# Performance work log

Measured on AMD Instinct MI355X. Metric: run time of the kernel, lower is better.

Reference implementation:

```python
import jax, jax.numpy as jnp
import numpy as np

N_NODES = 50000
N_EDGES = 600000
IN_CH = 128
OUT_CH = 64
HID = 2 * OUT_CH  # 128


def setup_inputs() -> dict:
    key = jax.random.key(0)
    k1, k2, k3, k4 = jax.random.split(key, 4)
    x = jax.random.normal(k1, (N_NODES, IN_CH), dtype=jnp.float32)
    edge_index = jax.random.randint(k2, (2, N_EDGES), 0, N_NODES, dtype=jnp.int64)
    # Glorot-style init scale for linear weights (PyG GCNConv default init)
    W1 = jax.random.normal(k3, (IN_CH, HID), dtype=jnp.float32) * (1.0 / np.sqrt(IN_CH))
    b1 = jnp.zeros((HID,), dtype=jnp.float32)
    W2 = jax.random.normal(k4, (HID, OUT_CH), dtype=jnp.float32) * (1.0 / np.sqrt(HID))
    b2 = jnp.zeros((OUT_CH,), dtype=jnp.float32)
    return {"x": x, "edge_index": edge_index, "W1": W1, "b1": b1, "W2": W2, "b2": b2}


def _gcn_norm(edge_index, n_nodes):
    # Add self loops, then symmetric normalization: norm_e = d^-1/2[src] * d^-1/2[dst]
    loop = jnp.arange(n_nodes, dtype=edge_index.dtype)
    src = jnp.concatenate([edge_index[0], loop])
    dst = jnp.concatenate([edge_index[1], loop])
    deg = jax.ops.segment_sum(jnp.ones_like(dst, dtype=jnp.float32), dst, num_segments=n_nodes)
    dinv = jnp.where(deg > 0, jax.lax.rsqrt(deg), 0.0)
    norm = dinv[src] * dinv[dst]  # [E + N]
    return src, dst, norm


def _gcn_conv(x, src, dst, norm, W, b, n_nodes):
    h = x @ W                      # [N, d_out]  dense transform first (PyG order)
    msg = h[src] * norm[:, None]   # gather + scale: [E+N, d_out]
    agg = jax.ops.segment_sum(msg, dst, num_segments=n_nodes)  # scatter-add
    return agg + b


def reference(x, edge_index, W1, b1, W2, b2):
    n = x.shape[0]
    src, dst, norm = _gcn_norm(edge_index, n)  # shared (cached=True in original)
    h = jax.nn.relu(_gcn_conv(x, src, dst, norm, W1, b1, n))
    return _gcn_conv(h, src, dst, norm, W2, b2, n)
```

## Files before the change

### kernel.cpp

```cpp
#include <hip/hip_runtime.h>


typedef __attribute__((ext_vector_type(8))) short short8;
typedef __attribute__((ext_vector_type(4))) float float4v;

constexpr int PB = 128;

static __device__ __forceinline__ ushort f2bf(float f) {
  union { float f; unsigned u; } c; c.f = f;
  unsigned u = c.u;
  return (ushort)((u + 0x7fffu + ((u >> 16) & 1u)) >> 16);
}
static __device__ __forceinline__ float bf2f(ushort h) {
  union { unsigned u; float f; } c; c.u = ((unsigned)h) << 16;
  return c.f;
}
static __device__ __forceinline__ float bfhi(unsigned packed) {
  union { unsigned u; float f; } c; c.u = packed & 0xffff0000u;
  return c.f;
}
static __device__ __forceinline__ float bflo(unsigned packed) {
  union { unsigned u; float f; } c; c.u = packed << 16;
  return c.f;
}

static __device__ __forceinline__ void wswz_tile(const float* __restrict__ W,
                                                 ushort* __restrict__ whi,
                                                 ushort* __restrict__ wlo,
                                                 int M, int tile, int lane) {
  int ntiles = M >> 4;
  int kt = tile / ntiles, nt = tile % ntiles;
  int colg = nt * 16 + (lane & 15);
  int krow = kt * 32 + (lane >> 4) * 8;
  size_t o = ((size_t)tile * 64 + lane) * 8;
#pragma unroll
  for (int j = 0; j < 8; j++) {
    float v = W[(size_t)(krow + j) * M + colg];
    ushort h = f2bf(v);
    whi[o + j] = h;
    wlo[o + j] = f2bf(v - bf2f(h));
  }
}

static __device__ __forceinline__ void lds_scan512(const int* __restrict__ g, int m,
                                                   int* __restrict__ base,
                                                   int* __restrict__ buf) {
  int t = threadIdx.x;
  int carry = 0;
  for (int b0 = 0; b0 < 512; b0 += 256) {
    int idx = b0 + t;
    int v = (idx < m) ? g[idx] : 0;
    buf[t] = v;
    __syncthreads();
    for (int off = 1; off < 256; off <<= 1) {
      int add = (t >= off) ? buf[t - off] : 0;
      __syncthreads();
      buf[t] += add;
      __syncthreads();
    }
    base[idx] = carry + buf[t] - v;
    carry += buf[255];
    __syncthreads();
  }
}

__global__ __launch_bounds__(256) void k_p1(const int* __restrict__ dst, int E, int EPB,
                                            int NBK, int* __restrict__ cnt_mat,
                                            const float* __restrict__ W1,
                                            ushort* __restrict__ w1hi,
                                            ushort* __restrict__ w1lo,
                                            const float* __restrict__ W2,
                                            ushort* __restrict__ w2hi,
                                            ushort* __restrict__ w2lo) {
  __shared__ int hist[512];
  int b = blockIdx.x, t = threadIdx.x;
  if (b >= PB) {
    int tile = (b - PB) * 4 + (t >> 6);
    int lane = t & 63;
    if (tile < 32) wswz_tile(W1, w1hi, w1lo, 128, tile, lane);
    else           wswz_tile(W2, w2hi, w2lo, 64, tile - 32, lane);
    return;
  }
  for (int k = t; k < NBK; k += 256) hist[k] = 0;
  __syncthreads();
  int start = b * EPB;
  int stop = min(E, start + EPB);
  for (int e = start + t * 4; e < stop; e += 1024) {
    if (e + 4 <= stop) {
      int4 d = *(const int4*)(dst + e);
      atomicAdd(&hist[d.x >> 7], 1);
      atomicAdd(&hist[d.y >> 7], 1);
      atomicAdd(&hist[d.z >> 7], 1);
      atomicAdd(&hist[d.w >> 7], 1);
    } else {
      for (int j = e; j < stop; j++) atomicAdd(&hist[dst[j] >> 7], 1);
    }
  }
  __syncthreads();
  for (int k = t; k < NBK; k += 256) cnt_mat[k * PB + b] = hist[k];
}

__global__ __launch_bounds__(256) void k_p2(int* __restrict__ cnt_mat,
                                            int* __restrict__ btot, int NBK,
                                            const float* __restrict__ Af32,
                                            const ushort* __restrict__ Whi,
                                            const ushort* __restrict__ Wlo,
                                            ushort* __restrict__ Cb, int n) {
  __shared__ int buf[256];
  int bid = blockIdx.x, t = threadIdx.x;
  if (bid < NBK) {
    int v = (t < PB) ? cnt_mat[bid * PB + t] : 0;
    buf[t] = v;
    __syncthreads();
#pragma unroll
    for (int off = 1; off < 256; off <<= 1) {
      int add = (t >= off) ? buf[t - off] : 0;
      __syncthreads();
      buf[t] += add;
      __syncthreads();
    }
    if (t < PB) cnt_mat[bid * PB + t] = buf[t] - v;
    if (t == 255) btot[bid] = buf[255];
    return;
  }
  constexpr int K = 128, M = 128, NT = M / 16;
  int lane = t & 63;
  int wv = t >> 6;
  int quad = lane >> 4, lo16 = lane & 15;
  int rowbase = (bid - NBK) * 64 + wv * 16;
  int arow = rowbase + lo16;
  bool arow_ok = arow < n;
  float4v acc[NT];
#pragma unroll
  for (int nt = 0; nt < NT; nt++) acc[nt] = (float4v){0.f, 0.f, 0.f, 0.f};
  for (int kt = 0; kt < 4; kt++) {
    short8 ahi, alo;
    float av[8];
    if (arow_ok) {
      const float* ap = Af32 + (size_t)arow * K + kt * 32 + quad * 8;
      float4 a0 = *(const float4*)ap;
      float4 a1 = *(const float4*)(ap + 4);
      av[0] = a0.x; av[1] = a0.y; av[2] = a0.z; av[3] = a0.w;
      av[4] = a1.x; av[5] = a1.y; av[6] = a1.z; av[7] = a1.w;
    } else {
#pragma unroll
      for (int j = 0; j < 8; j++) av[j] = 0.f;
    }
#pragma unroll
    for (int j = 0; j < 8; j++) {
      ushort h = f2bf(av[j]);
      ahi[j] = (short)h;
      alo[j] = (short)f2bf(av[j] - bf2f(h));
    }
    const ushort* ph = Whi + ((size_t)(kt * NT) * 64 + lane) * 8;
    const ushort* pl = Wlo + ((size_t)(kt * NT) * 64 + lane) * 8;
#pragma unroll
    for (int nt = 0; nt < NT; nt++) {
      short8 bhi = *(const short8*)(ph + nt * 512);
      short8 blo = *(const short8*)(pl + nt * 512);
      acc[nt] = __builtin_amdgcn_mfma_f32_16x16x32_bf16(ahi, bhi, acc[nt], 0, 0, 0);
      acc[nt] = __builtin_amdgcn_mfma_f32_16x16x32_bf16(alo, bhi, acc[nt], 0, 0, 0);
      acc[nt] = __builtin_amdgcn_mfma_f32_16x16x32_bf16(ahi, blo, acc[nt], 0, 0, 0);
    }
  }
#pragma unroll
  for (int nt = 0; nt < NT; nt++) {
#pragma unroll
    for (int r = 0; r < 4; r++) {
      int row = rowbase + quad * 4 + r;
      if (row < n) Cb[(size_t)row * M + nt * 16 + lo16] = f2bf(acc[nt][r]);
    }
  }
}

__global__ __launch_bounds__(256) void k_p3(const int* __restrict__ src,
                                            const int* __restrict__ dst, int E, int EPB,
                                            int NBK, const int* __restrict__ btot,
                                            const int* __restrict__ cnt_mat,
                                            unsigned* __restrict__ part) {
  __shared__ int buf[256];
  __shared__ int base[512];
  __shared__ int cur[512];
  int b = blockIdx.x, t = threadIdx.x;
  lds_scan512(btot, NBK, base, buf);
  for (int k = t; k < NBK; k += 256) cur[k] = base[k] + cnt_mat[k * PB + b];
  __syncthreads();
  int start = b * EPB, stop = min(E, start + EPB);
  for (int e = start + t * 4; e < stop; e += 1024) {
    if (e + 4 <= stop) {
      int4 s = *(const int4*)(src + e);
      int4 d = *(const int4*)(dst + e);
      int p;
      p = atomicAdd(&cur[d.x >> 7], 1); part[p] = (unsigned)s.x | ((unsigned)(d.x & 127) << 25);
      p = atomicAdd(&cur[d.y >> 7], 1); part[p] = (unsigned)s.y | ((unsigned)(d.y & 127) << 25);
      p = atomicAdd(&cur[d.z >> 7], 1); part[p] = (unsigned)s.z | ((unsigned)(d.z & 127) << 25);
      p = atomicAdd(&cur[d.w >> 7], 1); part[p] = (unsigned)s.w | ((unsigned)(d.w & 127) << 25);
    } else {
      for (int j = e; j < stop; j++) {
        int p2 = atomicAdd(&cur[dst[j] >> 7], 1);
        part[p2] = (unsigned)src[j] | ((unsigned)(dst[j] & 127) << 25);
      }
    }
  }
}

__global__ __launch_bounds__(256) void k_p4(const int* __restrict__ btot, int NBK,
                                            const unsigned* __restrict__ part,
                                            int* __restrict__ row_ptr,
                                            float* __restrict__ dinv,
                                            int* __restrict__ col, int n, int E) {
  __shared__ int buf[256];
  __shared__ int base[512];
  __shared__ int cnt[128];
  __shared__ int cur[128];
  int b = blockIdx.x, t = threadIdx.x;
  lds_scan512(btot, NBK, base, buf);
  int beg = base[b], end = base[b + 1];
  if (t < 128) cnt[t] = 0;
  __syncthreads();
  for (int e = beg + t; e < end; e += 256) atomicAdd(&cnt[part[e] >> 25], 1);
  __syncthreads();
  int v = (t < 128) ? cnt[t] : 0;
  buf[t] = v;
  __syncthreads();
#pragma unroll
  for (int off = 1; off < 256; off <<= 1) {
    int add = (t >= off) ? buf[t - off] : 0;
    __syncthreads();
    buf[t] += add;
    __syncthreads();
  }
  if (t < 128) {
    int excl = buf[t] - v;
    cur[t] = beg + excl;
    int node = b * 128 + t;
    if (node < n) {
      row_ptr[node] = beg + excl;
      dinv[node] = rsqrtf((float)(v + 1));
    }
  }
  if (b == 0 && t == 0) row_ptr[n] = E;
  __syncthreads();
  for (int e = beg + t; e < end; e += 256) {
    unsigned p = part[e];
    int pos = atomicAdd(&cur[p >> 25], 1);
    col[pos] = (int)(p & 0x01FFFFFFu);
  }
}

__global__ __launch_bounds__(256) void k_gemm2(const ushort* __restrict__ Ahi,
                                               const ushort* __restrict__ Alo,
                                               const ushort* __restrict__ Whi,
                                               const ushort* __restrict__ Wlo,
                                               ushort* __restrict__ Cb, int n) {
  constexpr int K = 128, M = 64, NT = M / 16;
  int lane = threadIdx.x & 63;
  int wv = threadIdx.x >> 6;
  int quad = lane >> 4, lo16 = lane & 15;
  int rowbase = blockIdx.x * 64 + wv * 16;
  int arow = rowbase + lo16;
  bool arow_ok = arow < n;
  float4v acc[NT];
#pragma unroll
  for (int nt = 0; nt < NT; nt++) acc[nt] = (float4v){0.f, 0.f, 0.f, 0.f};
  for (int kt = 0; kt < 4; kt++) {
    short8 ahi, alo;
    if (arow_ok) {
      size_t ao = (size_t)arow * K + kt * 32 + quad * 8;
      ahi = *(const short8*)(Ahi + ao);
      alo = *(const short8*)(Alo + ao);
    } else {
      ahi = (short8)0; alo = (short8)0;
    }
    const ushort* ph = Whi + ((size_t)(kt * NT) * 64 + lane) * 8;
    const ushort* pl = Wlo + ((size_t)(kt * NT) * 64 + lane) * 8;
#pragma unroll
    for (int nt = 0; nt < NT; nt++) {
      short8 bhi = *(const short8*)(ph + nt * 512);
      short8 blo = *(const short8*)(pl + nt * 512);
      acc[nt] = __builtin_amdgcn_mfma_f32_16x16x32_bf16(ahi, bhi, acc[nt], 0, 0, 0);
      acc[nt] = __builtin_amdgcn_mfma_f32_16x16x32_bf16(alo, bhi, acc[nt], 0, 0, 0);
      acc[nt] = __builtin_amdgcn_mfma_f32_16x16x32_bf16(ahi, blo, acc[nt], 0, 0, 0);
    }
  }
#pragma unroll
  for (int nt = 0; nt < NT; nt++) {
#pragma unroll
    for (int r = 0; r < 4; r++) {
      int row = rowbase + quad * 4 + r;
      if (row < n) Cb[(size_t)row * M + nt * 16 + lo16] = f2bf(acc[nt][r]);
    }
  }
}

template <int C, bool RELU, bool SPLIT>
__global__ __launch_bounds__(256) void k_agg(const ushort* __restrict__ Hb,
                                             const int* __restrict__ row_ptr,
                                             const int* __restrict__ col,
                                             const float* __restrict__ dinv,
                                             const float* __restrict__ bias,
                                             float* __restrict__ out,
                                             ushort* __restrict__ outhi,
                                             ushort* __restrict__ outlo, int n) {
  constexpr int VPL = C / 64;
  int lane = threadIdx.x & 63;
  int v = blockIdx.x * 4 + (threadIdx.x >> 6);
  if (v >= n) return;
  float dv = dinv[v];
  float acc0 = 0.f, acc1 = 0.f;
  auto loadp = [&](int s) -> unsigned {
    if (VPL == 2) return *(const unsigned*)(Hb + (size_t)s * C + lane * 2);
    else          return (unsigned)Hb[(size_t)s * C + lane];
  };
  {
    unsigned u = loadp(v);
    if (VPL == 2) { acc0 = dv * bflo(u); acc1 = dv * bfhi(u); }
    else          { acc0 = dv * bf2f((ushort)u); }
  }
  int beg = row_ptr[v], end = row_ptr[v + 1];
  for (int base = beg; base < end; base += 64) {
    int m = end - base;
    if (m > 64) m = 64;
    int sl = 0;
    float wl = 0.f;
    if (lane < m) {
      sl = col[base + lane];
      wl = dinv[sl];
    }
    int j = 0;
    for (; j + 8 <= m; j += 8) {
      int s[8]; float wq[8]; unsigned u[8];
#pragma unroll
      for (int q = 0; q < 8; q++) { s[q] = __shfl(sl, j + q); wq[q] = __shfl(wl, j + q); }
#pragma unroll
      for (int q = 0; q < 8; q++) u[q] = loadp(s[q]);
#pragma unroll
      for (int q = 0; q < 8; q++) {
        if (VPL == 2) {
          acc0 = fmaf(wq[q], bflo(u[q]), acc0);
          acc1 = fmaf(wq[q], bfhi(u[q]), acc1);
        } else {
          acc0 = fmaf(wq[q], bf2f((ushort)u[q]), acc0);
        }
      }
    }
    for (; j + 4 <= m; j += 4) {
      int s[4]; float wq[4]; unsigned u[4];
#pragma unroll
      for (int q = 0; q < 4; q++) { s[q] = __shfl(sl, j + q); wq[q] = __shfl(wl, j + q); }
#pragma unroll
      for (int q = 0; q < 4; q++) u[q] = loadp(s[q]);
#pragma unroll
      for (int q = 0; q < 4; q++) {
        if (VPL == 2) {
          acc0 = fmaf(wq[q], bflo(u[q]), acc0);
          acc1 = fmaf(wq[q], bfhi(u[q]), acc1);
        } else {
          acc0 = fmaf(wq[q], bf2f((ushort)u[q]), acc0);
        }
      }
    }
    for (; j < m; j++) {
      int s = __shfl(sl, j);
      float wv = __shfl(wl, j);
      unsigned u = loadp(s);
      if (VPL == 2) {
        acc0 = fmaf(wv, bflo(u), acc0);
        acc1 = fmaf(wv, bfhi(u), acc1);
      } else {
        acc0 = fmaf(wv, bf2f((ushort)u), acc0);
      }
    }
  }
  float r0 = fmaf(dv, acc0, bias[lane * VPL + 0]);
  if (RELU) r0 = fmaxf(r0, 0.f);
  if (VPL == 2) {
    float r1 = fmaf(dv, acc1, bias[lane * VPL + 1]);
    if (RELU) r1 = fmaxf(r1, 0.f);
    if (SPLIT) {
      ushort h0 = f2bf(r0), h1 = f2bf(r1);
      ushort l0 = f2bf(r0 - bf2f(h0)), l1 = f2bf(r1 - bf2f(h1));
      ((unsigned*)outhi)[(size_t)v * (C / 2) + lane] = (unsigned)h0 | ((unsigned)h1 << 16);
      ((unsigned*)outlo)[(size_t)v * (C / 2) + lane] = (unsigned)l0 | ((unsigned)l1 << 16);
    } else {
      *(float2*)&out[(size_t)v * C + lane * 2] = make_float2(r0, r1);
    }
  } else {
    if (SPLIT) {
      ushort h0 = f2bf(r0);
      outhi[(size_t)v * C + lane] = h0;
      outlo[(size_t)v * C + lane] = f2bf(r0 - bf2f(h0));
    } else {
      out[(size_t)v * C + lane] = r0;
    }
  }
}

extern "C" void kernel_launch(void* const* d_in, const int* in_sizes, int n_in,
                              void* d_out, int out_size, void* d_ws, size_t ws_size,
                              hipStream_t stream) {
  const float* x  = (const float*)d_in[0];
  const int*   ei = (const int*)d_in[1];
  const float* W1 = (const float*)d_in[2];
  const float* b1 = (const float*)d_in[3];
  const float* W2 = (const float*)d_in[4];
  const float* b2 = (const float*)d_in[5];
  int N = in_sizes[0] / 128;
  int E = in_sizes[1] / 2;
  const int* src = ei;
  const int* dst = ei + E;
  int NBK = (N + 127) / 128;
  int EPB = ((E + PB - 1) / PB + 3) & ~3;

  auto al = [](size_t v) { return (v + 255) & ~(size_t)255; };
  char* w = (char*)d_ws;
  int*      cnt_mat = (int*)w;      w += al((size_t)NBK * PB * 4);
  int*      btot    = (int*)w;      w += al((size_t)NBK * 4);
  unsigned* part    = (unsigned*)w; w += al((size_t)E * 4);
  int*      row_ptr = (int*)w;      w += al((size_t)(N + 1) * 4);
  float*    dinv    = (float*)w;    w += al((size_t)N * 4);
  int*      colv    = (int*)w;      w += al((size_t)E * 4);
  ushort*   h       = (ushort*)w;   w += al((size_t)N * 128 * 2);
  ushort*   h1hi    = (ushort*)w;   w += al((size_t)N * 128 * 2);
  ushort*   h1lo    = (ushort*)w;   w += al((size_t)N * 128 * 2);
  ushort*   h2      = (ushort*)w;   w += al((size_t)N * 64 * 2);
  ushort*   w1hi    = (ushort*)w;   w += al((size_t)128 * 128 * 2);
  ushort*   w1lo    = (ushort*)w;   w += al((size_t)128 * 128 * 2);
  ushort*   w2hi    = (ushort*)w;   w += al((size_t)128 * 64 * 2);
  ushort*   w2lo    = (ushort*)w;   w += al((size_t)128 * 64 * 2);
  float* out = (float*)d_out;

  int GB = (N + 63) / 64;

  k_p1<<<PB + 12, 256, 0, stream>>>(dst, E, EPB, NBK, cnt_mat,
                                    W1, w1hi, w1lo, W2, w2hi, w2lo);
  k_p2<<<NBK + GB, 256, 0, stream>>>(cnt_mat, btot, NBK, x, w1hi, w1lo, h, N);
  k_p3<<<PB, 256, 0, stream>>>(src, dst, E, EPB, NBK, btot, cnt_mat, part);
  k_p4<<<NBK, 256, 0, stream>>>(btot, NBK, part, row_ptr, dinv, colv, N, E);
  k_agg<128, true, true><<<(N + 3) / 4, 256, 0, stream>>>(h, row_ptr, colv, dinv, b1,
                                                          nullptr, h1hi, h1lo, N);
  k_gemm2<<<GB, 256, 0, stream>>>(h1hi, h1lo, w2hi, w2lo, h2, N);
  k_agg<64, false, false><<<(N + 3) / 4, 256, 0, stream>>>(h2, row_ptr, colv, dinv, b2,
                                                           out, nullptr, nullptr, N);
}
```

Measured before the change: 175.5 us.

## Fuse all GCN phases into one cooperative persistent kernel with grid syncs

Measured after the change: 614.7 us. 250% more time.

```diff
diff --git a/kernel.cpp b/kernel.cpp
--- a/kernel.cpp
+++ b/kernel.cpp
@@ -1,5 +1,8 @@
 #include <hip/hip_runtime.h>
-
+#include <hip/hip_cooperative_groups.h>
+
+
+namespace cg = cooperative_groups;
 
 typedef __attribute__((ext_vector_type(8))) short short8;
 typedef __attribute__((ext_vector_type(4))) float float4v;
@@ -23,6 +26,32 @@
   union { unsigned u; float f; } c; c.u = packed << 16;
   return c.f;
 }
+
+struct MegaParams {
+  const float* x;
+  const int* src;
+  const int* dst;
+  const float* W1;
+  const float* b1;
+  const float* W2;
+  const float* b2;
+  int N, E, NBK, EPB, GB, NAGG;
+  int* cnt_mat;
+  int* btot;
+  unsigned* part;
+  int* row_ptr;
+  float* dinv;
+  int* col;
+  ushort* h;
+  ushort* h1hi;
+  ushort* h1lo;
+  ushort* h2;
+  ushort* w1hi;
+  ushort* w1lo;
+  ushort* w2hi;
+  ushort* w2lo;
+  float* out;
+};
 
 static __device__ __forceinline__ void wswz_tile(const float* __restrict__ W,
                                                  ushort* __restrict__ whi,
@@ -64,72 +93,61 @@
   }
 }
 
-__global__ __launch_bounds__(256) void k_p1(const int* __restrict__ dst, int E, int EPB,
-                                            int NBK, int* __restrict__ cnt_mat,
-                                            const float* __restrict__ W1,
-                                            ushort* __restrict__ w1hi,
-                                            ushort* __restrict__ w1lo,
-                                            const float* __restrict__ W2,
-                                            ushort* __restrict__ w2hi,
-                                            ushort* __restrict__ w2lo) {
-  __shared__ int hist[512];
-  int b = blockIdx.x, t = threadIdx.x;
-  if (b >= PB) {
-    int tile = (b - PB) * 4 + (t >> 6);
+static __device__ void phase1_body(int bid, const MegaParams& P, int* smem) {
+  int t = threadIdx.x;
+  if (bid >= PB) {
+    int tile = (bid - PB) * 4 + (t >> 6);
     int lane = t & 63;
-    if (tile < 32) wswz_tile(W1, w1hi, w1lo, 128, tile, lane);
-    else           wswz_tile(W2, w2hi, w2lo, 64, tile - 32, lane);
+    if (tile < 32) wswz_tile(P.W1, P.w1hi, P.w1lo, 128, tile, lane);
+    else           wswz_tile(P.W2, P.w2hi, P.w2lo, 64, tile - 32, lane);
     return;
   }
-  for (int k = t; k < NBK; k += 256) hist[k] = 0;
-  __syncthreads();
-  int start = b * EPB;
-  int stop = min(E, start + EPB);
+  int* hist = smem;
+  for (int k = t; k < P.NBK; k += 256) hist[k] = 0;
+  __syncthreads();
+  int start = bid * P.EPB;
+  int stop = min(P.E, start + P.EPB);
   for (int e = start + t * 4; e < stop; e += 1024) {
     if (e + 4 <= stop) {
-      int4 d = *(const int4*)(dst + e);
+      int4 d = *(const int4*)(P.dst + e);
       atomicAdd(&hist[d.x >> 7], 1);
       atomicAdd(&hist[d.y >> 7], 1);
       atomicAdd(&hist[d.z >> 7], 1);
       atomicAdd(&hist[d.w >> 7], 1);
     } else {
-      for (int j = e; j < stop; j++) atomicAdd(&hist[dst[j] >> 7], 1);
-    }
-  }
-  __syncthreads();
-  for (int k = t; k < NBK; k += 256) cnt_mat[k * PB + b] = hist[k];
-}
-
-__global__ __launch_bounds__(256) void k_p2(int* __restrict__ cnt_mat,
-                                            int* __restrict__ btot, int NBK,
-                                            const float* __restrict__ Af32,
-                                            const ushort* __restrict__ Whi,
-                                            const ushort* __restrict__ Wlo,
-                                            ushort* __restrict__ Cb, int n) {
-  __shared__ int buf[256];
-  int bid = blockIdx.x, t = threadIdx.x;
-  if (bid < NBK) {
-    int v = (t < PB) ? cnt_mat[bid * PB + t] : 0;
-    buf[t] = v;
+      for (int j = e; j < stop; j++) atomicAdd(&hist[P.dst[j] >> 7], 1);
+    }
+  }
+  __syncthreads();
+  for (int k = t; k < P.NBK; k += 256) P.cnt_mat[k * PB + bid] = hist[k];
+}
+
+static __device__ void phase2_scan(int bid, const MegaParams& P, int* smem) {
+  int t = threadIdx.x;
+  int* buf = smem;
+  int v = (t < PB) ? P.cnt_mat[bid * PB + t] : 0;
+  buf[t] = v;
+  __syncthreads();
+#pragma unroll
+  for (int off = 1; off < 256; off <<= 1) {
+    int add = (t >= off) ? buf[t - off] : 0;
     __syncthreads();
-#pragma unroll
-    for (int off = 1; off < 256; off <<= 1) {
-      int add = (t >= off) ? buf[t - off] : 0;
-      __syncthreads();
-      buf[t] += add;
-      __syncthreads();
-    }
-    if (t < PB) cnt_mat[bid * PB + t] = buf[t] - v;
-    if (t == 255) btot[bid] = buf[255];
-    return;
-  }
+    buf[t] += add;
+    __syncthreads();
+  }
+  if (t < PB) P.cnt_mat[bid * PB + t] = buf[t] - v;
+  if (t == 255) P.btot[bid] = buf[255];
+}
+
+static __device__ void gemm1_block(int gb, const MegaParams& P) {
   constexpr int K = 128, M = 128, NT = M / 16;
+  int t = threadIdx.x;
   int lane = t & 63;
   int wv = t >> 6;
   int quad = lane >> 4, lo16 = lane & 15;
-  int rowbase = (bid - NBK) * 64 + wv * 16;
+  int rowbase = gb * 64 + wv * 16;
   int arow = rowbase + lo16;
-  bool arow_ok = arow < n;
+  bool arow_ok = arow < P.N;
   float4v acc[NT];
 #pragma unroll
   for (int nt = 0; nt < NT; nt++) acc[nt] = (float4v){0.f, 0.f, 0.f, 0.f};
@@ -137,7 +155,7 @@
     short8 ahi, alo;
     float av[8];
     if (arow_ok) {
-      const float* ap = Af32 + (size_t)arow * K + kt * 32 + quad * 8;
+      const float* ap = P.x + (size_t)arow * K + kt * 32 + quad * 8;
       float4 a0 = *(const float4*)ap;
       float4 a1 = *(const float4*)(ap + 4);
       av[0] = a0.x; av[1] = a0.y; av[2] = a0.z; av[3] = a0.w;
@@ -148,12 +166,12 @@
     }
 #pragma unroll
     for (int j = 0; j < 8; j++) {
-      ushort h = f2bf(av[j]);
-      ahi[j] = (short)h;
-      alo[j] = (short)f2bf(av[j] - bf2f(h));
-    }
-    const ushort* ph = Whi + ((size_t)(kt * NT) * 64 + lane) * 8;
-    const ushort* pl = Wlo + ((size_t)(kt * NT) * 64 + lane) * 8;
+      ushort hh = f2bf(av[j]);
+      ahi[j] = (short)hh;
+      alo[j] = (short)f2bf(av[j] - bf2f(hh));
+    }
+    const ushort* ph = P.w1hi + ((size_t)(kt * NT) * 64 + lane) * 8;
+    const ushort* pl = P.w1lo + ((size_t)(kt * NT) * 64 + lane) * 8;
 #pragma unroll
     for (int nt = 0; nt < NT; nt++) {
       short8 bhi = *(const short8*)(ph + nt * 512);
@@ -168,57 +186,49 @@
 #pragma unroll
     for (int r = 0; r < 4; r++) {
       int row = rowbase + quad * 4 + r;
-      if (row < n) Cb[(size_t)row * M + nt * 16 + lo16] = f2bf(acc[nt][r]);
-    }
-  }
-}
-
-__global__ __launch_bounds__(256) void k_p3(const int* __restrict__ src,
-                                            const int* __restrict__ dst, int E, int EPB,
-                                            int NBK, const int* __restrict__ btot,
-                                            const int* __restrict__ cnt_mat,
-                                            unsigned* __restrict__ part) {
-  __shared__ int buf[256];
-  __shared__ int base[512];
-  __shared__ int cur[512];
-  int b = blockIdx.x, t = threadIdx.x;
-  lds_scan512(btot, NBK, base, buf);
-  for (int k = t; k < NBK; k += 256) cur[k] = base[k] + cnt_mat[k * PB + b];
-  __syncthreads();
-  int start = b * EPB, stop = min(E, start + EPB);
+      if (row < P.N) P.h[(size_t)row * M + nt * 16 + lo16] = f2bf(acc[nt][r]);
+    }
+  }
+}
+
+static __device__ void phase3_body(int bid, const MegaParams& P, int* smem) {
+  int t = threadIdx.x;
+  int* buf = smem;
+  int* base = smem + 256;
+  int* cur = smem + 768;
+  lds_scan512(P.btot, P.NBK, base, buf);
+  for (int k = t; k < P.NBK; k += 256) cur[k] = base[k] + P.cnt_mat[k * PB + bid];
+  __syncthreads();
+  int start = bid * P.EPB, stop = min(P.E, start + P.EPB);
   for (int e = start + t * 4; e < stop; e += 1024) {
     if (e + 4 <= stop) {
-      int4 s = *(const int4*)(src + e);
-      int4 d = *(const int4*)(dst + e);
+      int4 s = *(const int4*)(P.src + e);
+      int4 d = *(const int4*)(P.dst + e);
       int p;
-      p = atomicAdd(&cur[d.x >> 7], 1); part[p] = (unsigned)s.x | ((unsigned)(d.x & 127) << 25);
-      p = atomicAdd(&cur[d.y >> 7], 1); part[p] = (unsigned)s.y | ((unsigned)(d.y & 127) << 25);
-      p = atomicAdd(&cur[d.z >> 7], 1); part[p] = (unsigned)s.z | ((unsigned)(d.z & 127) << 25);
-      p = atomicAdd(&cur[d.w >> 7], 1); part[p] = (unsigned)s.w | ((unsigned)(d.w & 127) << 25);
+      p = atomicAdd(&cur[d.x >> 7], 1); P.part[p] = (unsigned)s.x | ((unsigned)(d.x & 127) << 25);
+      p = atomicAdd(&cur[d.y >> 7], 1); P.part[p] = (unsigned)s.y | ((unsigned)(d.y & 127) << 25);
+      p = atomicAdd(&cur[d.z >> 7], 1); P.part[p] = (unsigned)s.z | ((unsigned)(d.z & 127) << 25);
+      p = atomicAdd(&cur[d.w >> 7], 1); P.part[p] = (unsigned)s.w | ((unsigned)(d.w & 127) << 25);
     } else {
       for (int j = e; j < stop; j++) {
-        int p2 = atomicAdd(&cur[dst[j] >> 7], 1);
-        part[p2] = (unsigned)src[j] | ((unsigned)(dst[j] & 127) << 25);
+        int p2 = atomicAdd(&cur[P.dst[j] >> 7], 1);
+        P.part[p2] = (unsigned)P.src[j] | ((unsigned)(P.dst[j] & 127) << 25);
       }
     }
   }
 }
 
-__global__ __launch_bounds__(256) void k_p4(const int* __restrict__ btot, int NBK,
-                                            const unsigned* __restrict__ part,
-                                            int* __restrict__ row_ptr,
-                                            float* __restrict__ dinv,
-                                            int* __restrict__ col, int n, int E) {
-  __shared__ int buf[256];
-  __shared__ int base[512];
-  __shared__ int cnt[128];
-  __shared__ int cur[128];
-  int b = blockIdx.x, t = threadIdx.x;
-  lds_scan512(btot, NBK, base, buf);
-  int beg = base[b], end = base[b + 1];
+static __device__ void phase4_body(int bid, const MegaParams& P, int* smem) {
+  int t = threadIdx.x;
+  int* buf = smem;
+  int* base = smem + 256;
+  int* cnt = smem + 768;
+  int* cur = smem + 896;
+  lds_scan512(P.btot, P.NBK, base, buf);
+  int beg = base[bid], end = base[bid + 1];
   if (t < 128) cnt[t] = 0;
   __syncthreads();
-  for (int e = beg + t; e < end; e += 256) atomicAdd(&cnt[part[e] >> 25], 1);
+  for (int e = beg + t; e < end; e += 256) atomicAdd(&cnt[P.part[e] >> 25], 1);
   __syncthreads();
   int v = (t < 128) ? cnt[t] : 0;
   buf[t] = v;
@@ -233,33 +243,30 @@
   if (t < 128) {
     int excl = buf[t] - v;
     cur[t] = beg + excl;
-    int node = b * 128 + t;
-    if (node < n) {
-      row_ptr[node] = beg + excl;
-      dinv[node] = rsqrtf((float)(v + 1));
-    }
-  }
-  if (b == 0 && t == 0) row_ptr[n] = E;
+    int node = bid * 128 + t;
+    if (node < P.N) {
+      P.row_ptr[node] = beg + excl;
+      P.dinv[node] = rsqrtf((float)(v + 1));
+    }
+  }
+  if (bid == 0 && t == 0) P.row_ptr[P.N] = P.E;
   __syncthreads();
   for (int e = beg + t; e < end; e += 256) {
-    unsigned p = part[e];
+    unsigned p = P.part[e];
     int pos = atomicAdd(&cur[p >> 25], 1);
-    col[pos] = (int)(p & 0x01FFFFFFu);
-  }
-}
-
-__global__ __launch_bounds__(256) void k_gemm2(const ushort* __restrict__ Ahi,
-                                               const ushort* __restrict__ Alo,
-                                               const ushort* __restrict__ Whi,
-                                               const ushort* __restrict__ Wlo,
-                                               ushort* __restrict__ Cb, int n) {
+    P.col[pos] = (int)(p & 0x01FFFFFFu);
+  }
+}
+
+static __device__ void gemm2_block(int gb, const MegaParams& P) {
   constexpr int K = 128, M = 64, NT = M / 16;
-  int lane = threadIdx.x & 63;
-  int wv = threadIdx.x >> 6;
+  int t = threadIdx.x;
+  int lane = t & 63;
+  int wv = t >> 6;
   int quad = lane >> 4, lo16 = lane & 15;
-  int rowbase = blockIdx.x * 64 + wv * 16;
+  int rowbase = gb * 64 + wv * 16;
   int arow = rowbase + lo16;
-  bool arow_ok = arow < n;
+  bool arow_ok = arow < P.N;
   float4v acc[NT];
 #pragma unroll
   for (int nt = 0; nt < NT; nt++) acc[nt] = (float4v){0.f, 0.f, 0.f, 0.f};
@@ -267,13 +274,13 @@
     short8 ahi, alo;
     if (arow_ok) {
       size_t ao = (size_t)arow * K + kt * 32 + quad * 8;
-      ahi = *(const short8*)(Ahi + ao);
-      alo = *(const short8*)(Alo + ao);
+      ahi = *(const short8*)(P.h1hi + ao);
+      alo = *(const short8*)(P.h1lo + ao);
     } else {
       ahi = (short8)0; alo = (short8)0;
     }
-    const ushort* ph = Whi + ((size_t)(kt * NT) * 64 + lane) * 8;
-    const ushort* pl = Wlo + ((size_t)(kt * NT) * 64 + lane) * 8;
+    const ushort* ph = P.w2hi + ((size_t)(kt * NT) * 64 + lane) * 8;
+    const ushort* pl = P.w2lo + ((size_t)(kt * NT) * 64 + lane) * 8;
 #pragma unroll
     for (int nt = 0; nt < NT; nt++) {
       short8 bhi = *(const short8*)(ph + nt * 512);
@@ -288,25 +295,23 @@
 #pragma unroll
     for (int r = 0; r < 4; r++) {
       int row = rowbase + quad * 4 + r;
-      if (row < n) Cb[(size_t)row * M + nt * 16 + lo16] = f2bf(acc[nt][r]);
+      if (row < P.N) P.h2[(size_t)row * M + nt * 16 + lo16] = f2bf(acc[nt][r]);
     }
   }
 }
 
 template <int C, bool RELU, bool SPLIT>
-__global__ __launch_bounds__(256) void k_agg(const ushort* __restrict__ Hb,
-                                             const int* __restrict__ row_ptr,
-                                             const int* __restrict__ col,
-                                             const float* __restrict__ dinv,
-                                             const float* __restrict__ bias,
-                                             float* __restrict__ out,
-                                             ushort* __restrict__ outhi,
-                                             ushort* __restrict__ outlo, int n) {
+static __device__ void agg_block(int vb, const MegaParams& P,
+                                 const ushort* __restrict__ Hb,
+                                 const float* __restrict__ bias,
+                                 float* __restrict__ out,
+                                 ushort* __restrict__ outhi,
+                                 ushort* __restrict__ outlo) {
   constexpr int VPL = C / 64;
   int lane = threadIdx.x & 63;
-  int v = blockIdx.x * 4 + (threadIdx.x >> 6);
-  if (v >= n) return;
-  float dv = dinv[v];
+  int v = vb * 4 + (threadIdx.x >> 6);
+  if (v >= P.N) return;
+  float dv = P.dinv[v];
   float acc0 = 0.f, acc1 = 0.f;
   auto loadp = [&](int s) -> unsigned {
     if (VPL == 2) return *(const unsigned*)(Hb + (size_t)s * C + lane * 2);
@@ -317,15 +322,15 @@
     if (VPL == 2) { acc0 = dv * bflo(u); acc1 = dv * bfhi(u); }
     else          { acc0 = dv * bf2f((ushort)u); }
   }
-  int beg = row_ptr[v], end = row_ptr[v + 1];
+  int beg = P.row_ptr[v], end = P.row_ptr[v + 1];
   for (int base = beg; base < end; base += 64) {
     int m = end - base;
     if (m > 64) m = 64;
     int sl = 0;
     float wl = 0.f;
     if (lane < m) {
-      sl = col[base + lane];
-      wl = dinv[sl];
+      sl = P.col[base + lane];
+      wl = P.dinv[sl];
     }
     int j = 0;
     for (; j + 8 <= m; j += 8) {
@@ -396,50 +401,116 @@
   }
 }
 
+__global__ __launch_bounds__(256, 4) void k_mega(MegaParams P) {
+  cg::grid_group grid = cg::this_grid();
+  __shared__ int smem[1280];
+  int bid = blockIdx.x;
+  int stride = gridDim.x;
+
+  for (int vb = bid; vb < PB + 12; vb += stride) { phase1_body(vb, P, smem); __syncthreads(); }
+  grid.sync();
+  for (int vb = bid; vb < P.NBK + P.GB; vb += stride) {
+    if (vb < P.NBK) { phase2_scan(vb, P, smem); __syncthreads(); }
+    else            gemm1_block(vb - P.NBK, P);
+  }
+  grid.sync();
+  for (int vb = bid; vb < PB; vb += stride) { phase3_body(vb, P, smem); __syncthreads(); }
+  grid.sync();
+  for (int vb = bid; vb < P.NBK; vb += stride) { phase4_body(vb, P, smem); __syncthreads(); }
+  grid.sync();
+  for (int vb = bid; vb < P.NAGG; vb += stride)
+    agg_block<128, true, true>(vb, P, P.h, P.b1, nullptr, P.h1hi, P.h1lo);
+  grid.sync();
+  for (int vb = bid; vb < P.GB; vb += stride) gemm2_block(vb, P);
+  grid.sync();
+  for (int vb = bid; vb < P.NAGG; vb += stride)
+    agg_block<64, false, false>(vb, P, P.h2, P.b2, P.out, nullptr, nullptr);
+}
+
+__global__ __launch_bounds__(256) void k_f1(MegaParams P) {
+  __shared__ int smem[1280];
+  phase1_body(blockIdx.x, P, smem);
+}
+__global__ __launch_bounds__(256) void k_f2(MegaParams P) {
+  __shared__ int smem[1280];
+  int bid = blockIdx.x;
+  if (bid < P.NBK) phase2_scan(bid, P, smem);
+  else             gemm1_block(bid - P.NBK, P);
+}
+__global__ __launch_bounds__(256) void k_f3(MegaParams P) {
+  __shared__ int smem[1280];
+  phase3_body(blockIdx.x, P, smem);
+}
+__global__ __launch_bounds__(256) void k_f4(MegaParams P) {
+  __shared__ int smem[1280];
+  phase4_body(blockIdx.x, P, smem);
+}
+__global__ __launch_bounds__(256) void k_f5(MegaParams P) {
+  agg_block<128, true, true>(blockIdx.x, P, P.h, P.b1, nullptr, P.h1hi, P.h1lo);
+}
+__global__ __launch_bounds__(256) void k_f6(MegaParams P) {
+  gemm2_block(blockIdx.x, P);
+}
+__global__ __launch_bounds__(256) void k_f7(MegaParams P) {
+  agg_block<64, false, false>(blockIdx.x, P, P.h2, P.b2, P.out, nullptr, nullptr);
+}
+
 extern "C" void kernel_launch(void* const* d_in, const int* in_sizes, int n_in,
                               void* d_out, int out_size, void* d_ws, size_t ws_size,
                               hipStream_t stream) {
-  const float* x  = (const float*)d_in[0];
-  const int*   ei = (const int*)d_in[1];
-  const float* W1 = (const float*)d_in[2];
-  const float* b1 = (const float*)d_in[3];
-  const float* W2 = (const float*)d_in[4];
-  const float* b2 = (const float*)d_in[5];
-  int N = in_sizes[0] / 128;
-  int E = in_sizes[1] / 2;
-  const int* src = ei;
-  const int* dst = ei + E;
-  int NBK = (N + 127) / 128;
-  int EPB = ((E + PB - 1) / PB + 3) & ~3;
+  MegaParams P;
+  P.x  = (const float*)d_in[0];
+  const int* ei = (const int*)d_in[1];
+  P.W1 = (const float*)d_in[2];
+  P.b1 = (const float*)d_in[3];
+  P.W2 = (const float*)d_in[4];
+  P.b2 = (const float*)d_in[5];
+  P.N = in_sizes[0] / 128;
+  P.E = in_sizes[1] / 2;
+  P.src = ei;
+  P.dst = ei + P.E;
+  P.NBK = (P.N + 127) / 128;
+  P.EPB = ((P.E + PB - 1) / PB + 3) & ~3;
+  P.GB = (P.N + 63) / 64;
+  P.NAGG = (P.N + 3) / 4;
 
   auto al = [](size_t v) { return (v + 255) & ~(size_t)255; };
   char* w = (char*)d_ws;
-  int*      cnt_mat = (int*)w;      w += al((size_t)NBK * PB * 4);
-  int*      btot    = (int*)w;      w += al((size_t)NBK * 4);
-  unsigned* part    = (unsigned*)w; w += al((size_t)E * 4);
-  int*      row_ptr = (int*)w;      w += al((size_t)(N + 1) * 4);
-  float*    dinv    = (float*)w;    w += al((size_t)N * 4);
-  int*      colv    = (int*)w;      w += al((size_t)E * 4);
-  ushort*   h       = (ushort*)w;   w += al((size_t)N * 128 * 2);
-  ushort*   h1hi    = (ushort*)w;   w += al((size_t)N * 128 * 2);
-  ushort*   h1lo    = (ushort*)w;   w += al((size_t)N * 128 * 2);
-  ushort*   h2      = (ushort*)w;   w += al((size_t)N * 64 * 2);
-  ushort*   w1hi    = (ushort*)w;   w += al((size_t)128 * 128 * 2);
-  ushort*   w1lo    = (ushort*)w;   w += al((size_t)128 * 128 * 2);
-  ushort*   w2hi    = (ushort*)w;   w += al((size_t)128 * 64 * 2);
-  ushort*   w2lo    = (ushort*)w;   w += al((size_t)128 * 64 * 2);
-  float* out = (float*)d_out;
-
-  int GB = (N + 63) / 64;
-
-  k_p1<<<PB + 12, 256, 0, stream>>>(dst, E, EPB, NBK, cnt_mat,
-                                    W1, w1hi, w1lo, W2, w2hi, w2lo);
-  k_p2<<<NBK + GB, 256, 0, stream>>>(cnt_mat, btot, NBK, x, w1hi, w1lo, h, N);
-  k_p3<<<PB, 256, 0, stream>>>(src, dst, E, EPB, NBK, btot, cnt_mat, part);
-  k_p4<<<NBK, 256, 0, stream>>>(btot, NBK, part, row_ptr, dinv, colv, N, E);
-  k_agg<128, true, true><<<(N + 3) / 4, 256, 0, stream>>>(h, row_ptr, colv, dinv, b1,
-                                                          nullptr, h1hi, h1lo, N);
-  k_gemm2<<<GB, 256, 0, stream>>>(h1hi, h1lo, w2hi, w2lo, h2, N);
-  k_agg<64, false, false><<<(N + 3) / 4, 256, 0, stream>>>(h2, row_ptr, colv, dinv, b2,
-                                                           out, nullptr, nullptr, N);
-}
+  P.cnt_mat = (int*)w;      w += al((size_t)P.NBK * PB * 4);
+  P.btot    = (int*)w;      w += al((size_t)P.NBK * 4);
+  P.part    = (unsigned*)w; w += al((size_t)P.E * 4);
+  P.row_ptr = (int*)w;      w += al((size_t)(P.N + 1) * 4);
+  P.dinv    = (float*)w;    w += al((size_t)P.N * 4);
+  P.col     = (int*)w;      w += al((size_t)P.E * 4);
+  P.h       = (ushort*)w;   w += al((size_t)P.N * 128 * 2);
+  P.h1hi    = (ushort*)w;   w += al((size_t)P.N * 128 * 2);
+  P.h1lo    = (ushort*)w;   w += al((size_t)P.N * 128 * 2);
+  P.h2      = (ushort*)w;   w += al((size_t)P.N * 64 * 2);
+  P.w1hi    = (ushort*)w;   w += al((size_t)128 * 128 * 2);
+  P.w1lo    = (ushort*)w;   w += al((size_t)128 * 128 * 2);
+  P.w2hi    = (ushort*)w;   w += al((size_t)128 * 64 * 2);
+  P.w2lo    = (ushort*)w;   w += al((size_t)128 * 64 * 2);
+  P.out = (float*)d_out;
+
+  hipError_t err = hipErrorUnknown;
+  int devId = 0, numCU = 0, maxBlk = 0;
+  if (hipGetDevice(&devId) == hipSuccess &&
+      hipDeviceGetAttribute(&numCU, hipDeviceAttributeMultiprocessorCount, devId) == hipSuccess &&
+      hipOccupancyMaxActiveBlocksPerMultiprocessor(&maxBlk, (const void*)k_mega, 256, 0) == hipSuccess &&
+      numCU > 0 && maxBlk > 0) {
+    int grid = numCU * maxBlk;
+    if (grid > 1024) grid = 1024;
+    void* kargs[] = {(void*)&P};
+    err = hipLaunchCooperativeKernel((const void*)k_mega, dim3(grid), dim3(256),
+                                     kargs, 0, stream);
+  }
+  if (err != hipSuccess) {
+    k_f1<<<PB + 12, 256, 0, stream>>>(P);
+    k_f2<<<P.NBK + P.GB, 256, 0, stream>>>(P);
+    k_f3<<<PB, 256, 0, stream>>>(P);
+    k_f4<<<P.NBK, 256, 0, stream>>>(P);
+    k_f5<<<P.NAGG, 256, 0, stream>>>(P);
+    k_f6<<<P.GB, 256, 0, stream>>>(P);
+    k_f7<<<P.NAGG, 256, 0, stream>>>(P);
+  }
+}
```
